# Performance work log

Measured on AMD Instinct MI355X. Metric: run time of the kernel, lower is better.

The kernel has to match this reference:

```python
import jax, jax.numpy as jnp
import numpy as np

N = 100000          # nodes
E = 3200000         # edges (avg degree 32)
D_IN = 64           # node_in
D_OUT = 64          # out_channels (heads=1)
NEG_SLOPE = 0.2     # PyG GATConv default
EPS = 1e-5          # BatchNorm eps


def setup_inputs() -> dict:
    key = jax.random.key(0)
    ks = jax.random.split(key, 6)
    node_feats = jax.random.normal(ks[0], (N, D_IN), dtype=jnp.float32)
    edge_index = jax.random.randint(ks[1], (2, E), 0, N, dtype=jnp.int64)
    W = jax.random.normal(ks[2], (D_IN, D_OUT), dtype=jnp.float32) / np.sqrt(D_IN)
    att_src = jax.random.normal(ks[3], (D_OUT,), dtype=jnp.float32) * 0.1
    att_dst = jax.random.normal(ks[4], (D_OUT,), dtype=jnp.float32) * 0.1
    bias = jnp.zeros((D_OUT,), dtype=jnp.float32)
    gamma = jnp.ones((D_OUT,), dtype=jnp.float32)
    beta = jnp.zeros((D_OUT,), dtype=jnp.float32)
    return {"node_feats": node_feats, "edge_index": edge_index, "W": W,
            "att_src": att_src, "att_dst": att_dst, "bias": bias,
            "gamma": gamma, "beta": beta}


def reference(node_feats, edge_index, W, att_src, att_dst, bias, gamma, beta):
    n = node_feats.shape[0]
    # Linear transform: (N, D_OUT)
    x = node_feats @ W
    # Add self-loops (PyG GATConv default add_self_loops=True)
    loops = jnp.arange(n, dtype=edge_index.dtype)
    src = jnp.concatenate([edge_index[0], loops])  # (E+N,)
    dst = jnp.concatenate([edge_index[1], loops])
    # Per-node attention logits, gathered per edge
    a_src = x @ att_src  # (N,)
    a_dst = x @ att_dst  # (N,)
    e = jax.nn.leaky_relu(a_src[src] + a_dst[dst], NEG_SLOPE)  # (E+N,)
    # Scatter-softmax over incoming edges of each destination node
    m = jax.ops.segment_max(e, dst, num_segments=n)
    ex = jnp.exp(e - m[dst])
    s = jax.ops.segment_sum(ex, dst, num_segments=n)
    alpha = ex / s[dst]  # (E+N,)
    # Weighted scatter-add aggregation of transformed source features
    out = jax.ops.segment_sum(x[src] * alpha[:, None], dst, num_segments=n) + bias
    # BatchNorm1d (training-mode batch statistics) + ReLU
    mu = out.mean(axis=0)
    var = out.var(axis=0)
    out = (out - mu) / jnp.sqrt(var + EPS) * gamma + beta
    return jax.nn.relu(out)
```

## Files before the change

### kernel.cpp

```cpp
#include <hip/hip_runtime.h>
#include <hip/hip_fp16.h>

#define NN 100000
#define NE 3200000
#define NEG_SLOPE 0.2f
#define BN_EPS 1e-5f
#define NBUK 196
#define CAP 17400
#define CHUNK 4096
#define NB_A 782

__device__ __forceinline__ unsigned short f2bf(float f) {
    unsigned u = __float_as_uint(f);
    return (unsigned short)((u + 0x7FFFu + ((u >> 16) & 1u)) >> 16);
}
__device__ __forceinline__ float bf2f(unsigned short h) {
    return __uint_as_float((unsigned)h << 16);
}
__device__ __forceinline__ float wdec(unsigned u) {
    return __half2float(__ushort_as_half((unsigned short)(u >> 17)));
}

__global__ __launch_bounds__(256) void init_kernel(const int* __restrict__ idx,
                                                   int* __restrict__ flag,
                                                   int* __restrict__ gcur,
                                                   float* __restrict__ stats) {
    int t = threadIdx.x;
    if (t < NBUK) gcur[t] = t * CAP;
    if (t < 128) stats[t] = 0.f;
    if (t == 0) {
        int any = 0;
#pragma unroll
        for (int k = 0; k < 16; ++k) any |= idx[2 * k + 1];
        *flag = (any == 0) ? 1 : 0;
    }
}

__global__ __launch_bounds__(256) void transform_kernel(
    const float* __restrict__ feats, const float* __restrict__ W,
    const float* __restrict__ att_s, const float* __restrict__ att_d,
    unsigned short* __restrict__ xb, float* __restrict__ a_src, float* __restrict__ a_dst) {
    int n = blockIdx.x * 256 + threadIdx.x;
    if (n >= NN) return;
    float acc[64];
#pragma unroll
    for (int j = 0; j < 64; ++j) acc[j] = 0.f;
    const float4* fr = (const float4*)(feats + (size_t)n * 64);
    for (int q = 0; q < 16; ++q) {
        float4 f = fr[q];
#pragma unroll
        for (int j = 0; j < 64; ++j) acc[j] = fmaf(f.x, W[(4 * q + 0) * 64 + j], acc[j]);
#pragma unroll
        for (int j = 0; j < 64; ++j) acc[j] = fmaf(f.y, W[(4 * q + 1) * 64 + j], acc[j]);
#pragma unroll
        for (int j = 0; j < 64; ++j) acc[j] = fmaf(f.z, W[(4 * q + 2) * 64 + j], acc[j]);
#pragma unroll
        for (int j = 0; j < 64; ++j) acc[j] = fmaf(f.w, W[(4 * q + 3) * 64 + j], acc[j]);
    }
    float as = 0.f, ad = 0.f;
#pragma unroll
    for (int j = 0; j < 64; ++j) {
        as = fmaf(acc[j], att_s[j], as);
        ad = fmaf(acc[j], att_d[j], ad);
    }
    unsigned w32[32];
#pragma unroll
    for (int j = 0; j < 32; ++j)
        w32[j] = (unsigned)f2bf(acc[2 * j]) | ((unsigned)f2bf(acc[2 * j + 1]) << 16);
    uint4* xr = (uint4*)(xb + (size_t)n * 64);
#pragma unroll
    for (int q = 0; q < 8; ++q)
        xr[q] = make_uint4(w32[4 * q], w32[4 * q + 1], w32[4 * q + 2], w32[4 * q + 3]);
    a_src[n] = as;
    a_dst[n] = ad;
}

__global__ __launch_bounds__(256) void binA_kernel(const int* __restrict__ idx,
                                                   const int* __restrict__ flag,
                                                   int* __restrict__ gcur,
                                                   unsigned* __restrict__ pairs) {
    __shared__ int hist[256];
    __shared__ int gbase[256];
    int t = threadIdx.x;
    int is64 = *flag;
    int c0 = blockIdx.x * CHUNK;
    int cnt = min(CHUNK, NE - c0);
    hist[t] = 0;
    __syncthreads();
    unsigned pk[16];
    int bks[16], rks[16];
#pragma unroll
    for (int k = 0; k < 16; ++k) {
        int j = t + k * 256;
        rks[k] = -1;
        if (j < cnt) {
            int i = c0 + j;
            int sn, dn;
            if (is64) { sn = idx[2 * (size_t)i]; dn = idx[2 * ((size_t)NE + i)]; }
            else      { sn = idx[i];             dn = idx[NE + i]; }
            int b = dn >> 9;
            bks[k] = b;
            pk[k] = ((unsigned)(dn & 511) << 17) | (unsigned)sn;
            rks[k] = atomicAdd(&hist[b], 1);
        }
    }
    __syncthreads();
    if (hist[t]) gbase[t] = atomicAdd(&gcur[t], hist[t]);
    __syncthreads();
#pragma unroll
    for (int k = 0; k < 16; ++k)
        if (rks[k] >= 0) {
            int pos = gbase[bks[k]] + rks[k];
            if (pos < (bks[k] + 1) * CAP) pairs[pos] = pk[k];
        }
}

__global__ __launch_bounds__(512) void sortB_kernel(const unsigned* __restrict__ pairs,
                                                    const int* __restrict__ gcur,
                                                    const float* __restrict__ a_src,
                                                    const float* __restrict__ a_dst,
                                                    int* __restrict__ row_ptr,
                                                    int* __restrict__ row_end,
                                                    unsigned* __restrict__ csr) {
    __shared__ int hist[512];
    __shared__ int curs[512];
    __shared__ float ads[512];
    int b = blockIdx.x;
    int t = threadIdx.x;
    int base = b * CAP, end = gcur[b];
    hist[t] = 0;
    int node = (b << 9) + t;
    ads[t] = (node < NN) ? a_dst[node] : 0.f;
    __syncthreads();
    for (int i = base + t; i < end; i += 512)
        atomicAdd(&hist[pairs[i] >> 17], 1);
    __syncthreads();
    int v = hist[t];
    for (int off = 1; off < 512; off <<= 1) {
        int add = (t >= off) ? hist[t - off] : 0;
        __syncthreads();
        hist[t] += add;
        __syncthreads();
    }
    int lofs = hist[t] - v;
    curs[t] = lofs;
    if (node < NN) {
        row_ptr[node] = base + lofs;
        row_end[node] = base + lofs + v;
    }
    __syncthreads();
    for (int i = base + t; i < end; i += 512) {
        unsigned u = pairs[i];
        int dl = u >> 17;
        int sn = (int)(u & 0x1FFFF);
        float e = a_src[sn] + ads[dl];
        e = fmaxf(e, NEG_SLOPE * e);
        float w = __expf(e);
        unsigned short hb = __half_as_ushort(__float2half(w));
        int pos = atomicAdd(&curs[dl], 1);
        csr[base + pos] = ((unsigned)hb << 17) | (unsigned)sn;
    }
}

__global__ __launch_bounds__(256) void aggregate_csr_kernel(
    const int* __restrict__ row_ptr, const int* __restrict__ row_end,
    const unsigned* __restrict__ csr, const unsigned short* __restrict__ xb,
    const float* __restrict__ a_src, const float* __restrict__ a_dst,
    float* __restrict__ out, float* __restrict__ stats) {
    int lane = threadIdx.x & 63;
    int w = threadIdx.x >> 6;
    int wid = blockIdx.x * 4 + w;
    int nw = gridDim.x * 4;
    float bn0 = 0.f, bn1 = 0.f;
    for (int n = wid; n < NN; n += nw) {
        int row0 = __builtin_amdgcn_readfirstlane(row_ptr[n]);
        int row1 = __builtin_amdgcn_readfirstlane(row_end[n]);
        float ad = a_dst[n];
        float es = a_src[n] + ad;
        es = fmaxf(es, NEG_SLOPE * es);
        float wself = __expf(es);
        float acc = wself * bf2f(xb[((size_t)n << 6) + lane]);
        float ssum = wself;
        int e = row0;
        for (; e + 8 <= row1; e += 8) {
            unsigned u0 = csr[e + 0], u1 = csr[e + 1], u2 = csr[e + 2], u3 = csr[e + 3];
            unsigned u4 = csr[e + 4], u5 = csr[e + 5], u6 = csr[e + 6], u7 = csr[e + 7];
            float v0 = bf2f(xb[(size_t)((u0 & 0x1FFFFu) << 6) + lane]);
            float v1 = bf2f(xb[(size_t)((u1 & 0x1FFFFu) << 6) + lane]);
            float v2 = bf2f(xb[(size_t)((u2 & 0x1FFFFu) << 6) + lane]);
            float v3 = bf2f(xb[(size_t)((u3 & 0x1FFFFu) << 6) + lane]);
            float v4 = bf2f(xb[(size_t)((u4 & 0x1FFFFu) << 6) + lane]);
            float v5 = bf2f(xb[(size_t)((u5 & 0x1FFFFu) << 6) + lane]);
            float v6 = bf2f(xb[(size_t)((u6 & 0x1FFFFu) << 6) + lane]);
            float v7 = bf2f(xb[(size_t)((u7 & 0x1FFFFu) << 6) + lane]);
            float w0 = wdec(u0), w1 = wdec(u1), w2 = wdec(u2), w3 = wdec(u3);
            float w4 = wdec(u4), w5 = wdec(u5), w6 = wdec(u6), w7 = wdec(u7);
            acc = fmaf(w0, v0, acc); acc = fmaf(w1, v1, acc);
            acc = fmaf(w2, v2, acc); acc = fmaf(w3, v3, acc);
            acc = fmaf(w4, v4, acc); acc = fmaf(w5, v5, acc);
            acc = fmaf(w6, v6, acc); acc = fmaf(w7, v7, acc);
            ssum += ((w0 + w1) + (w2 + w3)) + ((w4 + w5) + (w6 + w7));
        }
        for (; e < row1; ++e) {
            unsigned u = csr[e];
            float wv = wdec(u);
            acc = fmaf(wv, bf2f(xb[(size_t)((u & 0x1FFFFu) << 6) + lane]), acc);
            ssum += wv;
        }
        float o = acc * __builtin_amdgcn_rcpf(ssum);
        out[((size_t)n << 6) + lane] = o;
        bn0 += o;
        bn1 = fmaf(o, o, bn1);
    }
    __shared__ float l0[4][64], l1[4][64];
    l0[w][lane] = bn0;
    l1[w][lane] = bn1;
    __syncthreads();
    if (threadIdx.x < 64) {
        float t0 = l0[0][lane] + l0[1][lane] + l0[2][lane] + l0[3][lane];
        float t1 = l1[0][lane] + l1[1][lane] + l1[2][lane] + l1[3][lane];
        unsafeAtomicAdd(&stats[lane], t0);
        unsafeAtomicAdd(&stats[64 + lane], t1);
    }
}

__global__ __launch_bounds__(64) void bn_finalize_kernel(
    const float* __restrict__ stats, const float* __restrict__ gamma,
    const float* __restrict__ beta, float* __restrict__ coefs) {
    int c = threadIdx.x;
    if (c < 64) {
        float mu = stats[c] * (1.0f / NN);
        float var = stats[64 + c] * (1.0f / NN) - mu * mu;
        float sc = gamma[c] * rsqrtf(var + BN_EPS);
        coefs[c] = sc;
        coefs[64 + c] = fmaf(-mu, sc, beta[c]);
    }
}

__global__ __launch_bounds__(256) void bn_norm_kernel(float* __restrict__ out,
                                                      const float* __restrict__ coefs) {
    int stride = gridDim.x * 256;
    int total = NN * 16;
    for (int i = blockIdx.x * 256 + threadIdx.x; i < total; i += stride) {
        float4 v = ((const float4*)out)[i];
        int c = (i & 15) * 4;
        v.x = fmaxf(0.f, fmaf(v.x, coefs[c + 0], coefs[64 + c + 0]));
        v.y = fmaxf(0.f, fmaf(v.y, coefs[c + 1], coefs[64 + c + 1]));
        v.z = fmaxf(0.f, fmaf(v.z, coefs[c + 2], coefs[64 + c + 2]));
        v.w = fmaxf(0.f, fmaf(v.w, coefs[c + 3], coefs[64 + c + 3]));
        ((float4*)out)[i] = v;
    }
}

extern "C" void kernel_launch(void* const* d_in, const int* in_sizes, int n_in,
                              void* d_out, int out_size, void* d_ws, size_t ws_size,
                              hipStream_t stream) {
    const float* feats = (const float*)d_in[0];
    const int* idx     = (const int*)d_in[1];
    const float* W     = (const float*)d_in[2];
    const float* att_s = (const float*)d_in[3];
    const float* att_d = (const float*)d_in[4];
    const float* gamma = (const float*)d_in[6];
    const float* beta  = (const float*)d_in[7];
    float* out = (float*)d_out;

    unsigned short* xb = (unsigned short*)d_ws;
    float* a_src    = (float*)d_ws + (size_t)NN * 32;
    float* a_dst    = a_src + NN;
    int* gcur       = (int*)(a_dst + NN);
    int* row_ptr    = gcur + 256;
    int* row_end    = row_ptr + NN;
    unsigned* pairs = (unsigned*)(row_end + NN);
    unsigned* csr   = pairs + (size_t)NBUK * CAP;
    float* stats    = (float*)(csr + (size_t)NBUK * CAP);
    float* coefs    = stats + 128;
    int* flag       = (int*)(coefs + 128);

    init_kernel<<<1, 256, 0, stream>>>(idx, flag, gcur, stats);
    transform_kernel<<<(NN + 255) / 256, 256, 0, stream>>>(feats, W, att_s, att_d, xb, a_src, a_dst);
    binA_kernel<<<NB_A, 256, 0, stream>>>(idx, flag, gcur, pairs);
    sortB_kernel<<<NBUK, 512, 0, stream>>>(pairs, gcur, a_src, a_dst, row_ptr, row_end, csr);
    aggregate_csr_kernel<<<2048, 256, 0, stream>>>(row_ptr, row_end, csr, xb, a_src, a_dst, out, stats);
    bn_finalize_kernel<<<1, 64, 0, stream>>>(stats, gamma, beta, coefs);
    bn_norm_kernel<<<2048, 256, 0, stream>>>(out, coefs);
}
```

Baseline: 318.6 us.

## Drop init and BN-finalize kernels, widen aggregation gather to 16 edges

The single-thread init kernel becomes a memset: bucket cursors are now relative offsets, and each binning block detects the 64-bit index layout itself. The BN finalize kernel is folded into the normalize kernel, where each block computes scale and shift into shared memory. The aggregation loop now issues 16 CSR loads and 16 feature gathers per iteration, masking the tail by zeroing the weights. That raises memory-level parallelism but reads index entries past the row end, so some gathers go to arbitrary rows.

Result: faster. 311.1 us (-2.4%).

```diff
diff --git a/kernel.cpp b/kernel.cpp
--- a/kernel.cpp
+++ b/kernel.cpp
@@ -20,20 +20,11 @@
 __device__ __forceinline__ float wdec(unsigned u) {
     return __half2float(__ushort_as_half((unsigned short)(u >> 17)));
 }
-
-__global__ __launch_bounds__(256) void init_kernel(const int* __restrict__ idx,
-                                                   int* __restrict__ flag,
-                                                   int* __restrict__ gcur,
-                                                   float* __restrict__ stats) {
-    int t = threadIdx.x;
-    if (t < NBUK) gcur[t] = t * CAP;
-    if (t < 128) stats[t] = 0.f;
-    if (t == 0) {
-        int any = 0;
-#pragma unroll
-        for (int k = 0; k < 16; ++k) any |= idx[2 * k + 1];
-        *flag = (any == 0) ? 1 : 0;
-    }
+__device__ __forceinline__ int detect64(const int* __restrict__ idx) {
+    int any = 0;
+#pragma unroll
+    for (int k = 0; k < 16; ++k) any |= idx[2 * k + 1];
+    return any == 0;
 }
 
 __global__ __launch_bounds__(256) void transform_kernel(
@@ -76,13 +67,12 @@
 }
 
 __global__ __launch_bounds__(256) void binA_kernel(const int* __restrict__ idx,
-                                                   const int* __restrict__ flag,
                                                    int* __restrict__ gcur,
                                                    unsigned* __restrict__ pairs) {
     __shared__ int hist[256];
     __shared__ int gbase[256];
     int t = threadIdx.x;
-    int is64 = *flag;
+    int is64 = detect64(idx);
     int c0 = blockIdx.x * CHUNK;
     int cnt = min(CHUNK, NE - c0);
     hist[t] = 0;
@@ -96,8 +86,8 @@
         if (j < cnt) {
             int i = c0 + j;
             int sn, dn;
-            if (is64) { sn = idx[2 * (size_t)i]; dn = idx[2 * ((size_t)NE + i)]; }
-            else      { sn = idx[i];             dn = idx[NE + i]; }
+            if (is64) { sn = ((const int2*)idx)[i].x; dn = ((const int2*)idx)[(size_t)NE + i].x; }
+            else      { sn = idx[i];                  dn = idx[NE + i]; }
             int b = dn >> 9;
             bks[k] = b;
             pk[k] = ((unsigned)(dn & 511) << 17) | (unsigned)sn;
@@ -110,8 +100,8 @@
 #pragma unroll
     for (int k = 0; k < 16; ++k)
         if (rks[k] >= 0) {
-            int pos = gbase[bks[k]] + rks[k];
-            if (pos < (bks[k] + 1) * CAP) pairs[pos] = pk[k];
+            int rel = gbase[bks[k]] + rks[k];
+            if (rel < CAP) pairs[(size_t)bks[k] * CAP + rel] = pk[k];
         }
 }
 
@@ -127,7 +117,8 @@
     __shared__ float ads[512];
     int b = blockIdx.x;
     int t = threadIdx.x;
-    int base = b * CAP, end = gcur[b];
+    int base = b * CAP;
+    int end = base + min(gcur[b], CAP);
     hist[t] = 0;
     int node = (b << 9) + t;
     ads[t] = (node < NN) ? a_dst[node] : 0.f;
@@ -181,31 +172,20 @@
         float wself = __expf(es);
         float acc = wself * bf2f(xb[((size_t)n << 6) + lane]);
         float ssum = wself;
-        int e = row0;
-        for (; e + 8 <= row1; e += 8) {
-            unsigned u0 = csr[e + 0], u1 = csr[e + 1], u2 = csr[e + 2], u3 = csr[e + 3];
-            unsigned u4 = csr[e + 4], u5 = csr[e + 5], u6 = csr[e + 6], u7 = csr[e + 7];
-            float v0 = bf2f(xb[(size_t)((u0 & 0x1FFFFu) << 6) + lane]);
-            float v1 = bf2f(xb[(size_t)((u1 & 0x1FFFFu) << 6) + lane]);
-            float v2 = bf2f(xb[(size_t)((u2 & 0x1FFFFu) << 6) + lane]);
-            float v3 = bf2f(xb[(size_t)((u3 & 0x1FFFFu) << 6) + lane]);
-            float v4 = bf2f(xb[(size_t)((u4 & 0x1FFFFu) << 6) + lane]);
-            float v5 = bf2f(xb[(size_t)((u5 & 0x1FFFFu) << 6) + lane]);
-            float v6 = bf2f(xb[(size_t)((u6 & 0x1FFFFu) << 6) + lane]);
-            float v7 = bf2f(xb[(size_t)((u7 & 0x1FFFFu) << 6) + lane]);
-            float w0 = wdec(u0), w1 = wdec(u1), w2 = wdec(u2), w3 = wdec(u3);
-            float w4 = wdec(u4), w5 = wdec(u5), w6 = wdec(u6), w7 = wdec(u7);
-            acc = fmaf(w0, v0, acc); acc = fmaf(w1, v1, acc);
-            acc = fmaf(w2, v2, acc); acc = fmaf(w3, v3, acc);
-            acc = fmaf(w4, v4, acc); acc = fmaf(w5, v5, acc);
-            acc = fmaf(w6, v6, acc); acc = fmaf(w7, v7, acc);
-            ssum += ((w0 + w1) + (w2 + w3)) + ((w4 + w5) + (w6 + w7));
-        }
-        for (; e < row1; ++e) {
-            unsigned u = csr[e];
-            float wv = wdec(u);
-            acc = fmaf(wv, bf2f(xb[(size_t)((u & 0x1FFFFu) << 6) + lane]), acc);
-            ssum += wv;
+        for (int e = row0; e < row1; e += 16) {
+            unsigned u[16];
+#pragma unroll
+            for (int j = 0; j < 16; ++j) u[j] = csr[e + j];
+            float v[16];
+#pragma unroll
+            for (int j = 0; j < 16; ++j)
+                v[j] = bf2f(xb[((size_t)(u[j] & 0x1FFFFu) << 6) + lane]);
+#pragma unroll
+            for (int j = 0; j < 16; ++j) {
+                float wv = (e + j < row1) ? wdec(u[j]) : 0.f;
+                acc = fmaf(wv, v[j], acc);
+                ssum += wv;
+            }
         }
         float o = acc * __builtin_amdgcn_rcpf(ssum);
         out[((size_t)n << 6) + lane] = o;
@@ -224,30 +204,29 @@
     }
 }
 
-__global__ __launch_bounds__(64) void bn_finalize_kernel(
-    const float* __restrict__ stats, const float* __restrict__ gamma,
-    const float* __restrict__ beta, float* __restrict__ coefs) {
-    int c = threadIdx.x;
-    if (c < 64) {
-        float mu = stats[c] * (1.0f / NN);
-        float var = stats[64 + c] * (1.0f / NN) - mu * mu;
-        float sc = gamma[c] * rsqrtf(var + BN_EPS);
-        coefs[c] = sc;
-        coefs[64 + c] = fmaf(-mu, sc, beta[c]);
-    }
-}
-
 __global__ __launch_bounds__(256) void bn_norm_kernel(float* __restrict__ out,
-                                                      const float* __restrict__ coefs) {
+                                                      const float* __restrict__ stats,
+                                                      const float* __restrict__ gamma,
+                                                      const float* __restrict__ beta) {
+    __shared__ float sc[64], sh[64];
+    int t = threadIdx.x;
+    if (t < 64) {
+        float mu = stats[t] * (1.0f / NN);
+        float var = stats[64 + t] * (1.0f / NN) - mu * mu;
+        float s = gamma[t] * rsqrtf(var + BN_EPS);
+        sc[t] = s;
+        sh[t] = fmaf(-mu, s, beta[t]);
+    }
+    __syncthreads();
     int stride = gridDim.x * 256;
     int total = NN * 16;
-    for (int i = blockIdx.x * 256 + threadIdx.x; i < total; i += stride) {
+    for (int i = blockIdx.x * 256 + t; i < total; i += stride) {
         float4 v = ((const float4*)out)[i];
         int c = (i & 15) * 4;
-        v.x = fmaxf(0.f, fmaf(v.x, coefs[c + 0], coefs[64 + c + 0]));
-        v.y = fmaxf(0.f, fmaf(v.y, coefs[c + 1], coefs[64 + c + 1]));
-        v.z = fmaxf(0.f, fmaf(v.z, coefs[c + 2], coefs[64 + c + 2]));
-        v.w = fmaxf(0.f, fmaf(v.w, coefs[c + 3], coefs[64 + c + 3]));
+        v.x = fmaxf(0.f, fmaf(v.x, sc[c + 0], sh[c + 0]));
+        v.y = fmaxf(0.f, fmaf(v.y, sc[c + 1], sh[c + 1]));
+        v.z = fmaxf(0.f, fmaf(v.z, sc[c + 2], sh[c + 2]));
+        v.w = fmaxf(0.f, fmaf(v.w, sc[c + 3], sh[c + 3]));
         ((float4*)out)[i] = v;
     }
 }
@@ -268,19 +247,17 @@
     float* a_src    = (float*)d_ws + (size_t)NN * 32;
     float* a_dst    = a_src + NN;
     int* gcur       = (int*)(a_dst + NN);
-    int* row_ptr    = gcur + 256;
+    float* stats    = (float*)(gcur + 256);
+    int* row_ptr    = (int*)(stats + 128);
     int* row_end    = row_ptr + NN;
     unsigned* pairs = (unsigned*)(row_end + NN);
     unsigned* csr   = pairs + (size_t)NBUK * CAP;
-    float* stats    = (float*)(csr + (size_t)NBUK * CAP);
-    float* coefs    = stats + 128;
-    int* flag       = (int*)(coefs + 128);
-
-    init_kernel<<<1, 256, 0, stream>>>(idx, flag, gcur, stats);
+
+    hipMemsetAsync(gcur, 0, (256 + 128) * sizeof(int), stream);
+
     transform_kernel<<<(NN + 255) / 256, 256, 0, stream>>>(feats, W, att_s, att_d, xb, a_src, a_dst);
-    binA_kernel<<<NB_A, 256, 0, stream>>>(idx, flag, gcur, pairs);
+    binA_kernel<<<NB_A, 256, 0, stream>>>(idx, gcur, pairs);
     sortB_kernel<<<NBUK, 512, 0, stream>>>(pairs, gcur, a_src, a_dst, row_ptr, row_end, csr);
     aggregate_csr_kernel<<<2048, 256, 0, stream>>>(row_ptr, row_end, csr, xb, a_src, a_dst, out, stats);
-    bn_finalize_kernel<<<1, 64, 0, stream>>>(stats, gamma, beta, coefs);
-    bn_norm_kernel<<<2048, 256, 0, stream>>>(out, coefs);
-}
+    bn_norm_kernel<<<2048, 256, 0, stream>>>(out, stats, gamma, beta);
+}
```
